# Kernel tuning notes

Measured on AMD Instinct MI355X. Metric: run time of the kernel, lower is better.

## Reference

```python
import jax, jax.numpy as jnp
import numpy as np

DIM = 1024
N_HEADS = 16
HD = DIM // N_HEADS


def setup_inputs() -> dict:
    key = jax.random.key(0)
    k1, k2, k3 = jax.random.split(key, 3)
    x = jax.random.normal(k1, (4, 2048, DIM), dtype=jnp.float32)
    # torch nn.Linear weights: W_qkv [3*dim, dim], W_proj [dim, dim]; y = x @ W.T
    W_qkv = jax.random.normal(k2, (3 * DIM, DIM), dtype=jnp.float32) * 0.02
    W_proj = jax.random.normal(k3, (DIM, DIM), dtype=jnp.float32) * 0.02
    return {"x": x, "W_qkv": W_qkv, "W_proj": W_proj}


def reference(x, W_qkv, W_proj):
    B, T, D = x.shape
    H, hd = N_HEADS, HD
    # fused QKV projection: (B,T,3D)
    qkv = jnp.einsum('btd,ed->bte', x, W_qkv)
    # view(B,T,3,H,hd).transpose(1,2) -> (B,3,T,H,hd)
    qkv = qkv.reshape(B, T, 3, H, hd).transpose(0, 2, 1, 3, 4)
    q, k, v = qkv[:, 0], qkv[:, 1], qkv[:, 2]  # each (B,T,H,hd)
    # NOTE: faithful to source — SDPA sees (B,T) as batch dims and attends
    # over the heads axis (length H), NOT the sequence axis.
    scale = 1.0 / np.sqrt(hd).astype(np.float32)
    scores = jnp.einsum('btie,btje->btij', q, k) * scale  # (B,T,H,H)
    attn = jax.nn.softmax(scores, axis=-1)
    out = jnp.einsum('btij,btje->btie', attn, v)  # (B,T,H,hd)
    # out.transpose(1,2).contiguous().view(B,T,D)
    out = out.transpose(0, 2, 1, 3).reshape(B, T, D)
    return jnp.einsum('btd,ed->bte', out, W_proj)
```

## Files before the change

### kernel.cpp

```cpp
#include <hip/hip_runtime.h>


typedef __bf16 bf16x8 __attribute__((ext_vector_type(8)));
typedef float  f32x16 __attribute__((ext_vector_type(16)));

typedef __attribute__((address_space(3))) void       lds_void;
typedef const __attribute__((address_space(1))) void gbl_void;

__device__ __forceinline__ unsigned short f2b(float f) {
    unsigned int u = __builtin_bit_cast(unsigned int, f);
    return (unsigned short)((u + 0x7FFFu + ((u >> 16) & 1u)) >> 16);
}
__device__ __forceinline__ unsigned int pack2(float a, float b) {
    return (unsigned int)f2b(a) | ((unsigned int)f2b(b) << 16);
}
__device__ __forceinline__ void unpack8(uint4 u, float* f) {
    unsigned int w[4] = {u.x, u.y, u.z, u.w};
#pragma unroll
    for (int a = 0; a < 4; ++a) {
        union { unsigned int i; float f; } lo, hi;
        lo.i = w[a] << 16;
        hi.i = w[a] & 0xFFFF0000u;
        f[a * 2]     = lo.f;
        f[a * 2 + 1] = hi.f;
    }
}

__global__ __launch_bounds__(256) void cvt_all(const float* __restrict__ x,
                                               const float* __restrict__ wqkv,
                                               const float* __restrict__ wproj,
                                               unsigned short* __restrict__ xb,
                                               unsigned short* __restrict__ wqkvb,
                                               unsigned short* __restrict__ wprojb) {
    int i = blockIdx.x * 256 + threadIdx.x;
    const float* src;
    unsigned short* dst;
    if (i < 2097152)      { src = x;     dst = xb;                       }
    else if (i < 2883584) { src = wqkv;  dst = wqkvb;  i -= 2097152;     }
    else                  { src = wproj; dst = wprojb; i -= 2883584;     }
    float4 f = reinterpret_cast<const float4*>(src)[i];
    ushort4 u;
    u.x = f2b(f.x); u.y = f2b(f.y); u.z = f2b(f.z); u.w = f2b(f.w);
    reinterpret_cast<ushort4*>(dst)[i] = u;
}

__device__ __forceinline__ void store_c(float* C, long idx, float v)          { C[idx] = v; }
__device__ __forceinline__ void store_c(unsigned short* C, long idx, float v) { C[idx] = f2b(v); }

template <typename CT>
__global__ __launch_bounds__(256) void gemm_bt(const unsigned short* __restrict__ A,
                                               const unsigned short* __restrict__ B,
                                               CT* __restrict__ C,
                                               int M, int N, int K) {
    __shared__ __align__(16) unsigned short As[128 * 64];
    __shared__ __align__(16) unsigned short Bs[128 * 64];

    const int tid  = threadIdx.x;
    const int lane = tid & 63;
    const int wave = tid >> 6;
    const long bm  = blockIdx.y;
    const long bn  = blockIdx.x;
    const int wm   = (wave >> 1) * 64;
    const int wn   = (wave & 1) * 64;

    f32x16 acc[2][2] = {};

    const unsigned short* Ab = A + bm * 128 * (long)K;
    const unsigned short* Bb = B + bn * 128 * (long)K;

    const int srow  = tid >> 3;
    const int sgcol = ((tid & 7) ^ (srow & 7)) << 3;

    for (int k0 = 0; k0 < K; k0 += 64) {
#pragma unroll
        for (int r = 0; r < 4; ++r)
            __builtin_amdgcn_global_load_lds(
                (gbl_void*)(Ab + (long)(r * 32 + srow) * K + k0 + sgcol),
                (lds_void*)(As + (r * 256 + wave * 64) * 8), 16, 0, 0);
#pragma unroll
        for (int r = 0; r < 4; ++r)
            __builtin_amdgcn_global_load_lds(
                (gbl_void*)(Bb + (long)(r * 32 + srow) * K + k0 + sgcol),
                (lds_void*)(Bs + (r * 256 + wave * 64) * 8), 16, 0, 0);
        __syncthreads();

        const int arow = lane & 31;
        const int kh   = lane >> 5;
#pragma unroll
        for (int kk = 0; kk < 4; ++kk) {
            const int c  = kk * 2 + kh;
            const int sw = (c ^ (lane & 7)) << 3;
            bf16x8 af[2], bfr[2];
#pragma unroll
            for (int i = 0; i < 2; ++i)
                af[i] = *reinterpret_cast<const bf16x8*>(As + (wm + i * 32 + arow) * 64 + sw);
#pragma unroll
            for (int j = 0; j < 2; ++j)
                bfr[j] = *reinterpret_cast<const bf16x8*>(Bs + (wn + j * 32 + arow) * 64 + sw);
#pragma unroll
            for (int i = 0; i < 2; ++i)
#pragma unroll
                for (int j = 0; j < 2; ++j)
                    acc[i][j] = __builtin_amdgcn_mfma_f32_32x32x16_bf16(af[i], bfr[j], acc[i][j], 0, 0, 0);
        }
        __syncthreads();
    }

    const long mbase = bm * 128 + wm + ((lane >> 5) << 2);
    const long nbase = bn * 128 + wn + (lane & 31);
#pragma unroll
    for (int i = 0; i < 2; ++i)
#pragma unroll
        for (int j = 0; j < 2; ++j)
#pragma unroll
            for (int r = 0; r < 16; ++r) {
                const long row = mbase + i * 32 + (r & 3) + 8 * (r >> 2);
                store_c(C, row * (long)N + nbase + j * 32, acc[i][j][r]);
            }
}

__global__ __launch_bounds__(256) void attn_rowlocal(const unsigned short* __restrict__ qkv,
                                                     unsigned short* __restrict__ out3) {
    __shared__ __align__(16) unsigned short rows[4 * 3072];
    __shared__ float attnS[4][16][17];

    const int tid  = threadIdx.x;
    const int lane = tid & 63;
    const int wave = tid >> 6;
    const int m0   = blockIdx.x * 4;

    {
        const uint4* src = reinterpret_cast<const uint4*>(qkv + (long)m0 * 3072);
        uint4* dst = reinterpret_cast<uint4*>(rows);
#pragma unroll
        for (int c = 0; c < 6; ++c) {
            const int S  = c * 256 + tid;
            const int gs = (S & ~7) | ((S & 7) ^ ((S >> 3) & 7));
            dst[S] = src[gs];
        }
    }
    __syncthreads();

    const int m = m0 + wave;
    const int b = m >> 11;
    const int t = m & 2047;
    const unsigned short* rw = rows + wave * 3072;

    const int i  = lane & 15;
    const int j0 = (lane >> 4) << 2;
    float sc[4] = {0.f, 0.f, 0.f, 0.f};
#pragma unroll
    for (int c8 = 0; c8 < 8; ++c8) {
        uint4 qu = *reinterpret_cast<const uint4*>(rw + i * 64 + ((c8 ^ (i & 7)) << 3));
        float qf[8];
        unpack8(qu, qf);
#pragma unroll
        for (int jj = 0; jj < 4; ++jj) {
            const int vi = 16 + j0 + jj;
            uint4 ku = *reinterpret_cast<const uint4*>(rw + vi * 64 + ((c8 ^ (vi & 7)) << 3));
            float kf[8];
            unpack8(ku, kf);
#pragma unroll
            for (int d = 0; d < 8; ++d) sc[jj] += qf[d] * kf[d];
        }
    }
#pragma unroll
    for (int jj = 0; jj < 4; ++jj) sc[jj] *= 0.125f;

    float mx = fmaxf(fmaxf(sc[0], sc[1]), fmaxf(sc[2], sc[3]));
    mx = fmaxf(mx, __shfl_xor(mx, 16));
    mx = fmaxf(mx, __shfl_xor(mx, 32));
    float sum = 0.f;
#pragma unroll
    for (int jj = 0; jj < 4; ++jj) { sc[jj] = __expf(sc[jj] - mx); sum += sc[jj]; }
    sum += __shfl_xor(sum, 16);
    sum += __shfl_xor(sum, 32);
    const float inv = 1.0f / sum;
#pragma unroll
    for (int jj = 0; jj < 4; ++jj) attnS[wave][i][j0 + jj] = sc[jj] * inv;
    __syncthreads();

    const int oi = lane >> 2;
    const int s0 = (lane & 3) << 4;
    const int c0 = (lane & 3) << 1;
    float o[16];
#pragma unroll
    for (int s = 0; s < 16; ++s) o[s] = 0.f;
#pragma unroll
    for (int j = 0; j < 16; ++j) {
        const float a  = attnS[wave][oi][j];
        const int   vi = 32 + j;
        uint4 v0 = *reinterpret_cast<const uint4*>(rw + vi * 64 + (((c0)     ^ (vi & 7)) << 3));
        uint4 v1 = *reinterpret_cast<const uint4*>(rw + vi * 64 + (((c0 + 1) ^ (vi & 7)) << 3));
        float vf[16];
        unpack8(v0, vf);
        unpack8(v1, vf + 8);
#pragma unroll
        for (int s = 0; s < 16; ++s) o[s] += a * vf[s];
    }

    uint4 r0, r1;
    r0.x = pack2(o[0],  o[1]);  r0.y = pack2(o[2],  o[3]);
    r0.z = pack2(o[4],  o[5]);  r0.w = pack2(o[6],  o[7]);
    r1.x = pack2(o[8],  o[9]);  r1.y = pack2(o[10], o[11]);
    r1.z = pack2(o[12], o[13]); r1.w = pack2(o[14], o[15]);

    const long base = (long)b * (2048 * 1024)
                    + (long)(oi * 128 + (t >> 4)) * 1024
                    + 64 * (t & 15) + s0;
    *reinterpret_cast<uint4*>(out3 + base)     = r0;
    *reinterpret_cast<uint4*>(out3 + base + 8) = r1;
}

extern "C" void kernel_launch(void* const* d_in, const int* in_sizes, int n_in,
                              void* d_out, int out_size, void* d_ws, size_t ws_size,
                              hipStream_t stream) {
    const float* x     = (const float*)d_in[0];
    const float* Wqkv  = (const float*)d_in[1];
    const float* Wproj = (const float*)d_in[2];
    float* out = (float*)d_out;

    char* ws = (char*)d_ws;
    unsigned short* xb     = (unsigned short*)(ws);
    unsigned short* wqkvb  = (unsigned short*)(ws + 16777216);
    unsigned short* wprojb = (unsigned short*)(ws + 23068672);
    unsigned short* qkvb   = (unsigned short*)(ws + 25165824);
    unsigned short* out3b  = (unsigned short*)(ws + 75497472);

    cvt_all<<<dim3(12288), dim3(256), 0, stream>>>(x, Wqkv, Wproj, xb, wqkvb, wprojb);

    gemm_bt<unsigned short><<<dim3(24, 64), dim3(256), 0, stream>>>(
        xb, wqkvb, qkvb, 8192, 3072, 1024);

    attn_rowlocal<<<dim3(2048), dim3(256), 0, stream>>>(qkvb, out3b);

    gemm_bt<float><<<dim3(8, 64), dim3(256), 0, stream>>>(
        out3b, wprojb, out, 8192, 1024, 1024);
}
```

Baseline: 199.1 us.

## Register-prefetch next GEMM K-tile instead of direct global-to-LDS loads

The GEMM main loop no longer issues direct global-to-LDS loads followed by a barrier. It now prefetches the next 64-wide K tile into registers while the MFMA work on the current tile runs, then writes those registers to LDS after the second barrier. This is meant to hide global load latency behind compute. It costs extra VGPRs for the staging buffers and adds a redundant wrap-around load on the last iteration; the launch bound is also raised to request 3 blocks per SM.

```diff
diff --git a/kernel.cpp b/kernel.cpp
--- a/kernel.cpp
+++ b/kernel.cpp
@@ -3,9 +3,6 @@
 
 typedef __bf16 bf16x8 __attribute__((ext_vector_type(8)));
 typedef float  f32x16 __attribute__((ext_vector_type(16)));
-
-typedef __attribute__((address_space(3))) void       lds_void;
-typedef const __attribute__((address_space(1))) void gbl_void;
 
 __device__ __forceinline__ unsigned short f2b(float f) {
     unsigned int u = __builtin_bit_cast(unsigned int, f);
@@ -35,9 +32,9 @@
     int i = blockIdx.x * 256 + threadIdx.x;
     const float* src;
     unsigned short* dst;
-    if (i < 2097152)      { src = x;     dst = xb;                       }
-    else if (i < 2883584) { src = wqkv;  dst = wqkvb;  i -= 2097152;     }
-    else                  { src = wproj; dst = wprojb; i -= 2883584;     }
+    if (i < 2097152)      { src = x;     dst = xb;                   }
+    else if (i < 2883584) { src = wqkv;  dst = wqkvb;  i -= 2097152; }
+    else                  { src = wproj; dst = wprojb; i -= 2883584; }
     float4 f = reinterpret_cast<const float4*>(src)[i];
     ushort4 u;
     u.x = f2b(f.x); u.y = f2b(f.y); u.z = f2b(f.z); u.w = f2b(f.w);
@@ -48,10 +45,10 @@
 __device__ __forceinline__ void store_c(unsigned short* C, long idx, float v) { C[idx] = f2b(v); }
 
 template <typename CT>
-__global__ __launch_bounds__(256) void gemm_bt(const unsigned short* __restrict__ A,
-                                               const unsigned short* __restrict__ B,
-                                               CT* __restrict__ C,
-                                               int M, int N, int K) {
+__global__ __launch_bounds__(256, 3) void gemm_bt(const unsigned short* __restrict__ A,
+                                                  const unsigned short* __restrict__ B,
+                                                  CT* __restrict__ C,
+                                                  int M, int N, int K) {
     __shared__ __align__(16) unsigned short As[128 * 64];
     __shared__ __align__(16) unsigned short Bs[128 * 64];
 
@@ -65,24 +62,30 @@
 
     f32x16 acc[2][2] = {};
 
-    const unsigned short* Ab = A + bm * 128 * (long)K;
-    const unsigned short* Bb = B + bn * 128 * (long)K;
-
     const int srow  = tid >> 3;
     const int sgcol = ((tid & 7) ^ (srow & 7)) << 3;
 
+    const unsigned short* aptr = A + bm * 128 * (long)K + (long)srow * K + sgcol;
+    const unsigned short* bptr = B + bn * 128 * (long)K + (long)srow * K + sgcol;
+
+    uint4 areg[4], breg[4];
+#pragma unroll
+    for (int r = 0; r < 4; ++r) areg[r] = *reinterpret_cast<const uint4*>(aptr + (long)r * 32 * K);
+#pragma unroll
+    for (int r = 0; r < 4; ++r) breg[r] = *reinterpret_cast<const uint4*>(bptr + (long)r * 32 * K);
+#pragma unroll
+    for (int r = 0; r < 4; ++r) *reinterpret_cast<uint4*>(As + (r * 256 + tid) * 8) = areg[r];
+#pragma unroll
+    for (int r = 0; r < 4; ++r) *reinterpret_cast<uint4*>(Bs + (r * 256 + tid) * 8) = breg[r];
+
     for (int k0 = 0; k0 < K; k0 += 64) {
-#pragma unroll
-        for (int r = 0; r < 4; ++r)
-            __builtin_amdgcn_global_load_lds(
-                (gbl_void*)(Ab + (long)(r * 32 + srow) * K + k0 + sgcol),
-                (lds_void*)(As + (r * 256 + wave * 64) * 8), 16, 0, 0);
-#pragma unroll
-        for (int r = 0; r < 4; ++r)
-            __builtin_amdgcn_global_load_lds(
-                (gbl_void*)(Bb + (long)(r * 32 + srow) * K + k0 + sgcol),
-                (lds_void*)(Bs + (r * 256 + wave * 64) * 8), 16, 0, 0);
         __syncthreads();
+
+        const int kload = (k0 + 64 < K) ? (k0 + 64) : 0;
+#pragma unroll
+        for (int r = 0; r < 4; ++r) areg[r] = *reinterpret_cast<const uint4*>(aptr + (long)r * 32 * K + kload);
+#pragma unroll
+        for (int r = 0; r < 4; ++r) breg[r] = *reinterpret_cast<const uint4*>(bptr + (long)r * 32 * K + kload);
 
         const int arow = lane & 31;
         const int kh   = lane >> 5;
@@ -104,6 +107,11 @@
                     acc[i][j] = __builtin_amdgcn_mfma_f32_32x32x16_bf16(af[i], bfr[j], acc[i][j], 0, 0, 0);
         }
         __syncthreads();
+
+#pragma unroll
+        for (int r = 0; r < 4; ++r) *reinterpret_cast<uint4*>(As + (r * 256 + tid) * 8) = areg[r];
+#pragma unroll
+        for (int r = 0; r < 4; ++r) *reinterpret_cast<uint4*>(Bs + (r * 256 + tid) * 8) = breg[r];
     }
 
     const long mbase = bm * 128 + wm + ((lane >> 5) << 2);
@@ -185,7 +193,7 @@
     const int c0 = (lane & 3) << 1;
     float o[16];
 #pragma unroll
-    for (int s = 0; s < 16; ++s) o[s] = 0.f;
+    for (int ss = 0; ss < 16; ++ss) o[ss] = 0.f;
 #pragma unroll
     for (int j = 0; j < 16; ++j) {
         const float a  = attnS[wave][oi][j];
@@ -196,7 +204,7 @@
         unpack8(v0, vf);
         unpack8(v1, vf + 8);
 #pragma unroll
-        for (int s = 0; s < 16; ++s) o[s] += a * vf[s];
+        for (int ss = 0; ss < 16; ++ss) o[ss] += a * vf[ss];
     }
 
     uint4 r0, r1;
```

New measurement: 460.7 us. 2.31x slower.
